# Kernel tuning notes

Hardware: AMD Instinct MI355X
Metric: run time of the kernel (lower is better)

Reference implementation:

```python
import jax, jax.numpy as jnp
import numpy as np

B, C, H, W = 8, 64, 256, 256
K = 3  # num_experts in CondConv2D


def setup_inputs() -> dict:
    key = jax.random.key(0)
    ks = jax.random.split(key, 10)
    s = 0.05
    return {
        "x":    jax.random.normal(ks[0], (B, C, H, W), jnp.float32),
        # CondConv2D #1: depthwise 5x5, pad 2, dil 1
        "w0":   jax.random.normal(ks[1], (K, C, 1, 5, 5), jnp.float32) * s,
        "b0":   jax.random.normal(ks[2], (C,), jnp.float32) * s,
        "r0_w": jax.random.normal(ks[3], (K, C), jnp.float32) * s,
        "r0_b": jnp.zeros((K,), jnp.float32),
        # CondConv2D #2: depthwise 7x7, pad 9, dil 3
        "w1":   jax.random.normal(ks[4], (K, C, 1, 7, 7), jnp.float32) * s,
        "b1":   jax.random.normal(ks[5], (C,), jnp.float32) * s,
        "r1_w": jax.random.normal(ks[6], (K, C), jnp.float32) * s,
        "r1_b": jnp.zeros((K,), jnp.float32),
        # conv1: 1x1 pointwise
        "wp":   jax.random.normal(ks[7], (C, C), jnp.float32) * s,
        "bp":   jnp.zeros((C,), jnp.float32),
    }


def cond_dwconv(x, weight, bias, rw, rb, pad, dil):
    """Per-sample expert-mixed depthwise conv (CondConv with groups=C).
    x: [B,C,H,W]; weight: [K,C,1,ks,ks]; rw: [K,C], rb: [K]."""
    b, c, h, w = x.shape
    pooled = x.mean(axis=(2, 3))                      # [B,C] adaptive avg pool to 1x1
    r = jax.nn.sigmoid(pooled @ rw.T + rb)            # [B,K] routing weights
    wk = jnp.einsum('bk,kcihw->bcihw', r, weight)     # [B,C,1,ks,ks] mixed kernels
    ksz = weight.shape[-1]
    # batch-folded grouped conv: fold B into channel/group dim
    out = jax.lax.conv_general_dilated(
        x.reshape(1, b * c, h, w),
        wk.reshape(b * c, 1, ksz, ksz),
        window_strides=(1, 1),
        padding=[(pad, pad), (pad, pad)],
        rhs_dilation=(dil, dil),
        feature_group_count=b * c,
        dimension_numbers=('NCHW', 'OIHW', 'NCHW'))
    return out.reshape(b, c, h, w) + bias[None, :, None, None]


def reference(x, w0, b0, r0_w, r0_b, w1, b1, r1_w, r1_b, wp, bp):
    attn = jax.nn.gelu(cond_dwconv(x, w0, b0, r0_w, r0_b, pad=2, dil=1), approximate=False)
    attn = jax.nn.gelu(cond_dwconv(attn, w1, b1, r1_w, r1_b, pad=9, dil=3), approximate=False)
    attn = jnp.einsum('bchw,oc->bohw', attn, wp) + bp[None, :, None, None]  # 1x1 conv
    return x * attn
```

## Files before the change

### kernel.cpp

```cpp
#include <hip/hip_runtime.h>
#include <hip/hip_fp16.h>

#define HW 65536
#define PW 256
#define C7S 168

__device__ __forceinline__ float gelu_f(float v) {
    float ax = fabsf(v) * 0.7071067811865476f;
    float t  = 1.0f / (1.0f + 0.3275911f * ax);
    float p  = t * (0.254829592f + t * (-0.284496736f + t * (1.421413741f
             + t * (-1.453152027f + t * 1.061405429f))));
    float e  = 1.0f - p * __expf(-ax * ax);
    e = copysignf(e, v);
    return 0.5f * v * (1.0f + e);
}

__device__ __forceinline__ unsigned pack2h(float a, float b) {
    __half2 h = __floats2half2_rn(a, b);
    return *reinterpret_cast<unsigned*>(&h);
}

__device__ __forceinline__ void unpack8(uint4 u, float* dst) {
    float2 f;
    f = __half22float2(*reinterpret_cast<__half2*>(&u.x)); dst[0] = f.x; dst[1] = f.y;
    f = __half22float2(*reinterpret_cast<__half2*>(&u.y)); dst[2] = f.x; dst[3] = f.y;
    f = __half22float2(*reinterpret_cast<__half2*>(&u.z)); dst[4] = f.x; dst[5] = f.y;
    f = __half22float2(*reinterpret_cast<__half2*>(&u.w)); dst[6] = f.x; dst[7] = f.y;
}

__device__ __forceinline__ float sgpr_f(float v) {
    union { float f; int i; } u;
    u.f = v;
    u.i = __builtin_amdgcn_readfirstlane(u.i);
    return u.f;
}

__device__ __forceinline__ void fma_mix_h(float& acc, float w, unsigned h2, int sel) {
    if (sel == 0)
        asm("v_fma_mix_f32 %0, %1, %2, %0 op_sel:[0,0,0] op_sel_hi:[0,1,0]"
            : "+v"(acc) : "v"(w), "v"(h2));
    else
        asm("v_fma_mix_f32 %0, %1, %2, %0 op_sel:[0,1,0] op_sel_hi:[0,1,0]"
            : "+v"(acc) : "v"(w), "v"(h2));
}

__global__ __launch_bounds__(256) void k_pool_x(const float* __restrict__ x,
                                                float* __restrict__ partial) {
    __shared__ float red[256];
    const int t = threadIdx.x;
    const int blk = blockIdx.x;
    const float* p = x + (size_t)blk * 16384;
    float s = 0.f;
    #pragma unroll
    for (int i = 0; i < 16; ++i) {
        float4 v = *reinterpret_cast<const float4*>(p + (i * 256 + t) * 4);
        s += v.x + v.y + v.z + v.w;
    }
    red[t] = s;
    __syncthreads();
    for (int off = 128; off > 0; off >>= 1) {
        if (t < off) red[t] += red[t + off];
        __syncthreads();
    }
    if (t == 0) partial[blk] = red[0];
}

__global__ __launch_bounds__(64) void k_route_mix(const float* __restrict__ partial,
                                                  const float* __restrict__ rw,
                                                  const float* __restrict__ rb,
                                                  const float* __restrict__ wexp,
                                                  float* __restrict__ wkout,
                                                  int taps, int parts) {
    __shared__ float pool_s[64];
    __shared__ float r_s[3];
    const int b = blockIdx.x, c = threadIdx.x;
    float s = 0.f;
    for (int q = 0; q < parts; ++q) s += partial[(b * 64 + c) * parts + q];
    pool_s[c] = s * (1.0f / 65536.0f);
    __syncthreads();
    if (c < 3) {
        float z = rb[c];
        #pragma unroll
        for (int i = 0; i < 64; ++i) z += pool_s[i] * rw[c * 64 + i];
        r_s[c] = 1.0f / (1.0f + expf(-z));
    }
    __syncthreads();
    const float r0 = r_s[0], r1 = r_s[1], r2 = r_s[2];
    for (int j = 0; j < taps; ++j) {
        wkout[(b * 64 + c) * taps + j] =
            r0 * wexp[(0 * 64 + c) * taps + j] +
            r1 * wexp[(1 * 64 + c) * taps + j] +
            r2 * wexp[(2 * 64 + c) * taps + j];
    }
}

__global__ __launch_bounds__(256) void k_conv5(const float* __restrict__ x,
                                               const float* __restrict__ wk,
                                               const float* __restrict__ bias,
                                               __half* __restrict__ attn0,
                                               float* __restrict__ tilesum) {
    __shared__ float red[256];
    const int blk = blockIdx.x;
    const int plane = blk >> 2;
    const int tile = blk & 3;
    const int c = plane & 63;
    const int oy0 = (tile >> 1) << 7;
    const int ox0 = (tile & 1) << 7;
    const int t = threadIdx.x;
    const int ox = ox0 + ((t & 15) << 3);
    const int oy = oy0 + ((t >> 4) << 3);
    const float* xp = x + (size_t)plane * HW;
    const float* wkp = wk + plane * 25;
    float w[25];
    #pragma unroll
    for (int i = 0; i < 25; ++i) w[i] = sgpr_f(wkp[i]);
    float acc[8][8];
    #pragma unroll
    for (int i = 0; i < 8; ++i)
        #pragma unroll
        for (int j = 0; j < 8; ++j) acc[i][j] = 0.f;

    #pragma unroll
    for (int r = 0; r < 12; ++r) {
        const int gy = oy - 2 + r;
        if (gy >= 0 && gy < 256) {
            const float* rp = xp + gy * PW + ox;
            float buf[16];
            float4 v;
            if (ox > 0) v = *reinterpret_cast<const float4*>(rp - 4);
            else        v = make_float4(0.f, 0.f, 0.f, 0.f);
            buf[0] = v.x; buf[1] = v.y; buf[2] = v.z; buf[3] = v.w;
            v = *reinterpret_cast<const float4*>(rp);
            buf[4] = v.x; buf[5] = v.y; buf[6] = v.z; buf[7] = v.w;
            v = *reinterpret_cast<const float4*>(rp + 4);
            buf[8] = v.x; buf[9] = v.y; buf[10] = v.z; buf[11] = v.w;
            if (ox < 248) v = *reinterpret_cast<const float4*>(rp + 8);
            else          v = make_float4(0.f, 0.f, 0.f, 0.f);
            buf[12] = v.x; buf[13] = v.y; buf[14] = v.z; buf[15] = v.w;
            #pragma unroll
            for (int i = 0; i < 8; ++i) {
                const int d = r - i;
                if (d >= 0 && d <= 4) {
                    #pragma unroll
                    for (int dx = 0; dx < 5; ++dx) {
                        const float wv = w[d * 5 + dx];
                        #pragma unroll
                        for (int j = 0; j < 8; ++j)
                            acc[i][j] += wv * buf[j + dx + 2];
                    }
                }
            }
        }
    }
    const float bs = bias[c];
    float lsum = 0.f;
    __half* op = attn0 + (size_t)plane * HW;
    #pragma unroll
    for (int i = 0; i < 8; ++i) {
        float g[8];
        #pragma unroll
        for (int j = 0; j < 8; ++j) {
            g[j] = gelu_f(acc[i][j] + bs);
            lsum += g[j];
        }
        uint4 st;
        st.x = pack2h(g[0], g[1]); st.y = pack2h(g[2], g[3]);
        st.z = pack2h(g[4], g[5]); st.w = pack2h(g[6], g[7]);
        *reinterpret_cast<uint4*>(op + (oy + i) * PW + ox) = st;
    }
    red[t] = lsum;
    __syncthreads();
    for (int off = 128; off > 0; off >>= 1) {
        if (t < off) red[t] += red[t + off];
        __syncthreads();
    }
    if (t == 0) tilesum[blk] = red[0];
}

__global__ __launch_bounds__(256) void k_conv7(const __half* __restrict__ a0,
                                               const float* __restrict__ wk,
                                               const float* __restrict__ bias,
                                               __half* __restrict__ attn1) {
    __shared__ __half lds[82 * C7S];
    const int blk = blockIdx.x;
    const int plane = blk >> 3;
    const int tile = blk & 7;
    const int c = plane & 63;
    const int oy0 = (tile >> 1) << 6;
    const int ox0 = (tile & 1) << 7;
    const int t = threadIdx.x;
    const __half* ap = a0 + (size_t)plane * HW;

    const uint4 z4 = make_uint4(0u, 0u, 0u, 0u);
    #pragma unroll
    for (int it = 0; it < 7; ++it) {
        const int idx = it * 256 + t;
        if (idx < 1722) {
            const int lr = idx / 21;
            const int c8 = idx - lr * 21;
            const int gy = oy0 - 9 + lr;
            const int gx = ox0 - 16 + (c8 << 3);
            uint4 v = z4;
            if ((unsigned)gy < 256u && (unsigned)gx < 256u)
                v = *reinterpret_cast<const uint4*>(ap + gy * PW + gx);
            *reinterpret_cast<uint4*>(&lds[lr * C7S + (c8 << 3)]) = v;
        }
    }

    float w[49];
    #pragma unroll
    for (int i = 0; i < 49; ++i) w[i] = sgpr_f(wk[plane * 49 + i]);
    __syncthreads();

    const int tx = t & 3, ty = t >> 2;
    const int ox = tx << 5;
    float acc[32];
    #pragma unroll
    for (int j = 0; j < 32; ++j) acc[j] = 0.f;

    #pragma unroll
    for (int dyi = 0; dyi < 7; ++dyi) {
        const int lr = ty + 3 * dyi;
        const __half* lp = &lds[lr * C7S + ox];
        unsigned hbuf[32];
        #pragma unroll
        for (int k = 0; k < 8; ++k)
            *reinterpret_cast<uint4*>(&hbuf[k << 2]) =
                *reinterpret_cast<const uint4*>(lp + (k << 3));
        #pragma unroll
        for (int dxi = 0; dxi < 7; ++dxi) {
            const float wv = w[dyi * 7 + dxi];
            const int o = 7 + 3 * dxi;
            #pragma unroll
            for (int j = 0; j < 32; ++j) {
                const int h = o + j;
                fma_mix_h(acc[j], wv, hbuf[h >> 1], h & 1);
            }
        }
    }

    const float bs = bias[c];
    __half* op = attn1 + (size_t)plane * HW + (size_t)(oy0 + ty) * PW + ox0 + ox;
    #pragma unroll
    for (int q = 0; q < 4; ++q) {
        float g[8];
        #pragma unroll
        for (int j = 0; j < 8; ++j) g[j] = gelu_f(acc[q * 8 + j] + bs);
        uint4 st;
        st.x = pack2h(g[0], g[1]); st.y = pack2h(g[2], g[3]);
        st.z = pack2h(g[4], g[5]); st.w = pack2h(g[6], g[7]);
        *reinterpret_cast<uint4*>(op + (q << 3)) = st;
    }
}

__global__ __launch_bounds__(256) void k_mix(const __half* __restrict__ attn1,
                                             const float* __restrict__ wpm,
                                             const float* __restrict__ bp,
                                             const float* __restrict__ x,
                                             float* __restrict__ out) {
    __shared__ __half A_s[64][256];
    __shared__ float wpT[64][64];
    const int t = threadIdx.x;
    const int blk = blockIdx.x;
    const int b = blk >> 8;
    const int p0g = (blk & 255) << 8;
    #pragma unroll
    for (int it = 0; it < 8; ++it) {
        const int ci = it * 256 + t;
        const int row = ci >> 5;
        const int off = (ci & 31) << 3;
        uint4 u = *reinterpret_cast<const uint4*>(attn1 + (size_t)(b * 64 + row) * HW + p0g + off);
        *reinterpret_cast<uint4*>(&A_s[row][off]) = u;
    }
    #pragma unroll
    for (int j = 0; j < 16; ++j) {
        const int idx = j * 256 + t;
        const int cc = idx & 63;
        const int oo = idx >> 6;
        wpT[cc][oo] = wpm[oo * 64 + cc];
    }
    __syncthreads();
    const int o0 = (t >> 5) << 3;
    const int p0 = (t & 31) << 3;
    float acc[8][8];
    #pragma unroll
    for (int i = 0; i < 8; ++i)
        #pragma unroll
        for (int j = 0; j < 8; ++j) acc[i][j] = 0.f;
    #pragma unroll 4
    for (int cc = 0; cc < 64; ++cc) {
        float4 wa = *reinterpret_cast<const float4*>(&wpT[cc][o0]);
        float4 wb = *reinterpret_cast<const float4*>(&wpT[cc][o0 + 4]);
        const float wv[8] = {wa.x, wa.y, wa.z, wa.w, wb.x, wb.y, wb.z, wb.w};
        float af[8];
        uint4 u = *reinterpret_cast<const uint4*>(&A_s[cc][p0]);
        unpack8(u, af);
        #pragma unroll
        for (int oo = 0; oo < 8; ++oo) {
            const float wvv = wv[oo];
            #pragma unroll
            for (int pp = 0; pp < 8; ++pp) acc[oo][pp] += wvv * af[pp];
        }
    }
    #pragma unroll
    for (int oo = 0; oo < 8; ++oo) {
        const int o = o0 + oo;
        const float bb = bp[o];
        const size_t base = (size_t)(b * 64 + o) * HW + p0g + p0;
        float4 x0 = *reinterpret_cast<const float4*>(x + base);
        float4 x1 = *reinterpret_cast<const float4*>(x + base + 4);
        float4 r0, r1;
        r0.x = x0.x * (acc[oo][0] + bb); r0.y = x0.y * (acc[oo][1] + bb);
        r0.z = x0.z * (acc[oo][2] + bb); r0.w = x0.w * (acc[oo][3] + bb);
        r1.x = x1.x * (acc[oo][4] + bb); r1.y = x1.y * (acc[oo][5] + bb);
        r1.z = x1.z * (acc[oo][6] + bb); r1.w = x1.w * (acc[oo][7] + bb);
        *reinterpret_cast<float4*>(out + base) = r0;
        *reinterpret_cast<float4*>(out + base + 4) = r1;
    }
}

extern "C" void kernel_launch(void* const* d_in, const int* in_sizes, int n_in,
                              void* d_out, int out_size, void* d_ws, size_t ws_size,
                              hipStream_t stream) {
    const float* x   = (const float*)d_in[0];
    const float* w0  = (const float*)d_in[1];
    const float* b0  = (const float*)d_in[2];
    const float* r0w = (const float*)d_in[3];
    const float* r0b = (const float*)d_in[4];
    const float* w1  = (const float*)d_in[5];
    const float* b1  = (const float*)d_in[6];
    const float* r1w = (const float*)d_in[7];
    const float* r1b = (const float*)d_in[8];
    const float* wpm = (const float*)d_in[9];
    const float* bp  = (const float*)d_in[10];
    float* out = (float*)d_out;

    char* ws = (char*)d_ws;
    __half* attn0   = (__half*)(ws);
    __half* attn1   = (__half*)(ws + 67108864);
    float* partial0 = (float*)(ws + 134217728);
    float* tilesum1 = (float*)(ws + 134217728 + 8192);
    float* wk0      = (float*)(ws + 134217728 + 16384);
    float* wk1      = (float*)(ws + 134217728 + 16384 + 51200);

    k_pool_x<<<2048, 256, 0, stream>>>(x, partial0);
    k_route_mix<<<8, 64, 0, stream>>>(partial0, r0w, r0b, w0, wk0, 25, 4);
    k_conv5<<<2048, 256, 0, stream>>>(x, wk0, b0, attn0, tilesum1);
    k_route_mix<<<8, 64, 0, stream>>>(tilesum1, r1w, r1b, w1, wk1, 49, 4);
    k_conv7<<<4096, 256, 0, stream>>>(attn0, wk1, b1, attn1);
    k_mix<<<2048, 256, 0, stream>>>(attn1, wpm, bp, x, out);
}
```

Before: 266.8 us.

## Fuse routing/kernel-mix into conv kernels and pad conv7 LDS row stride

Removes the two small k_route_mix launches. Each conv block now recomputes the routing sigmoid and its own mixed depthwise kernel in shared memory from the pooled partial sums. This saves launch overhead and the tiny serial kernels between the big ones, at the cost of redundant routing work and extra barriers in every block. The conv7 LDS tile is also restrided to 85 dwords per row with word-granular stores and loads, aimed at reducing bank conflicts, but it gives up 128-bit LDS accesses.

New measurement: 257.2 us. 3.6% less time.

```diff
diff --git a/kernel.cpp b/kernel.cpp
--- a/kernel.cpp
+++ b/kernel.cpp
@@ -3,7 +3,7 @@
 
 #define HW 65536
 #define PW 256
-#define C7S 168
+#define C7SD 85
 
 __device__ __forceinline__ float gelu_f(float v) {
     float ax = fabsf(v) * 0.7071067811865476f;
@@ -65,44 +65,50 @@
     if (t == 0) partial[blk] = red[0];
 }
 
-__global__ __launch_bounds__(64) void k_route_mix(const float* __restrict__ partial,
-                                                  const float* __restrict__ rw,
-                                                  const float* __restrict__ rb,
-                                                  const float* __restrict__ wexp,
-                                                  float* __restrict__ wkout,
-                                                  int taps, int parts) {
-    __shared__ float pool_s[64];
-    __shared__ float r_s[3];
-    const int b = blockIdx.x, c = threadIdx.x;
-    float s = 0.f;
-    for (int q = 0; q < parts; ++q) s += partial[(b * 64 + c) * parts + q];
-    pool_s[c] = s * (1.0f / 65536.0f);
-    __syncthreads();
-    if (c < 3) {
-        float z = rb[c];
-        #pragma unroll
-        for (int i = 0; i < 64; ++i) z += pool_s[i] * rw[c * 64 + i];
-        r_s[c] = 1.0f / (1.0f + expf(-z));
-    }
-    __syncthreads();
-    const float r0 = r_s[0], r1 = r_s[1], r2 = r_s[2];
-    for (int j = 0; j < taps; ++j) {
-        wkout[(b * 64 + c) * taps + j] =
-            r0 * wexp[(0 * 64 + c) * taps + j] +
-            r1 * wexp[(1 * 64 + c) * taps + j] +
-            r2 * wexp[(2 * 64 + c) * taps + j];
-    }
+__device__ __forceinline__ void route_block(const float* __restrict__ partial,
+                                            const float* __restrict__ rw,
+                                            const float* __restrict__ rb,
+                                            const float* __restrict__ wexp,
+                                            int b, int c, int taps, int t,
+                                            float* pool_s, float* r_s, float* w_s) {
+    if (t < 64) {
+        float s = 0.f;
+        #pragma unroll
+        for (int q = 0; q < 4; ++q) s += partial[(b * 64 + t) * 4 + q];
+        pool_s[t] = s * (1.0f / 65536.0f);
+    }
+    __syncthreads();
+    if (t < 3) {
+        float z = rb[t];
+        #pragma unroll
+        for (int i = 0; i < 64; ++i) z += pool_s[i] * rw[t * 64 + i];
+        r_s[t] = 1.0f / (1.0f + expf(-z));
+    }
+    __syncthreads();
+    if (t < taps) {
+        w_s[t] = r_s[0] * wexp[(0 * 64 + c) * taps + t] +
+                 r_s[1] * wexp[(1 * 64 + c) * taps + t] +
+                 r_s[2] * wexp[(2 * 64 + c) * taps + t];
+    }
+    __syncthreads();
 }
 
 __global__ __launch_bounds__(256) void k_conv5(const float* __restrict__ x,
-                                               const float* __restrict__ wk,
+                                               const float* __restrict__ partial,
+                                               const float* __restrict__ rw,
+                                               const float* __restrict__ rb,
+                                               const float* __restrict__ wexp,
                                                const float* __restrict__ bias,
                                                __half* __restrict__ attn0,
                                                float* __restrict__ tilesum) {
     __shared__ float red[256];
+    __shared__ float pool_s[64];
+    __shared__ float r_s[3];
+    __shared__ float w_s[25];
     const int blk = blockIdx.x;
     const int plane = blk >> 2;
     const int tile = blk & 3;
+    const int b = plane >> 6;
     const int c = plane & 63;
     const int oy0 = (tile >> 1) << 7;
     const int ox0 = (tile & 1) << 7;
@@ -110,10 +116,12 @@
     const int ox = ox0 + ((t & 15) << 3);
     const int oy = oy0 + ((t >> 4) << 3);
     const float* xp = x + (size_t)plane * HW;
-    const float* wkp = wk + plane * 25;
+
+    route_block(partial, rw, rb, wexp, b, c, 25, t, pool_s, r_s, w_s);
     float w[25];
     #pragma unroll
-    for (int i = 0; i < 25; ++i) w[i] = sgpr_f(wkp[i]);
+    for (int i = 0; i < 25; ++i) w[i] = sgpr_f(w_s[i]);
+
     float acc[8][8];
     #pragma unroll
     for (int i = 0; i < 8; ++i)
@@ -178,13 +186,20 @@
 }
 
 __global__ __launch_bounds__(256) void k_conv7(const __half* __restrict__ a0,
-                                               const float* __restrict__ wk,
+                                               const float* __restrict__ tilesum,
+                                               const float* __restrict__ rw,
+                                               const float* __restrict__ rb,
+                                               const float* __restrict__ wexp,
                                                const float* __restrict__ bias,
                                                __half* __restrict__ attn1) {
-    __shared__ __half lds[82 * C7S];
+    __shared__ unsigned lds[82 * C7SD];
+    __shared__ float pool_s[64];
+    __shared__ float r_s[3];
+    __shared__ float w_s[49];
     const int blk = blockIdx.x;
     const int plane = blk >> 3;
     const int tile = blk & 7;
+    const int b = plane >> 6;
     const int c = plane & 63;
     const int oy0 = (tile >> 1) << 6;
     const int ox0 = (tile & 1) << 7;
@@ -203,13 +218,15 @@
             uint4 v = z4;
             if ((unsigned)gy < 256u && (unsigned)gx < 256u)
                 v = *reinterpret_cast<const uint4*>(ap + gy * PW + gx);
-            *reinterpret_cast<uint4*>(&lds[lr * C7S + (c8 << 3)]) = v;
-        }
-    }
-
+            unsigned* wp = &lds[lr * C7SD + (c8 << 2)];
+            wp[0] = v.x; wp[1] = v.y; wp[2] = v.z; wp[3] = v.w;
+        }
+    }
+
+    route_block(tilesum, rw, rb, wexp, b, c, 49, t, pool_s, r_s, w_s);
     float w[49];
     #pragma unroll
-    for (int i = 0; i < 49; ++i) w[i] = sgpr_f(wk[plane * 49 + i]);
+    for (int i = 0; i < 49; ++i) w[i] = sgpr_f(w_s[i]);
     __syncthreads();
 
     const int tx = t & 3, ty = t >> 2;
@@ -221,12 +238,10 @@
     #pragma unroll
     for (int dyi = 0; dyi < 7; ++dyi) {
         const int lr = ty + 3 * dyi;
-        const __half* lp = &lds[lr * C7S + ox];
+        const unsigned* lp = &lds[lr * C7SD + (tx << 4)];
         unsigned hbuf[32];
         #pragma unroll
-        for (int k = 0; k < 8; ++k)
-            *reinterpret_cast<uint4*>(&hbuf[k << 2]) =
-                *reinterpret_cast<const uint4*>(lp + (k << 3));
+        for (int i = 0; i < 32; ++i) hbuf[i] = lp[i];
         #pragma unroll
         for (int dxi = 0; dxi < 7; ++dxi) {
             const float wv = w[dyi * 7 + dxi];
@@ -340,13 +355,9 @@
     __half* attn1   = (__half*)(ws + 67108864);
     float* partial0 = (float*)(ws + 134217728);
     float* tilesum1 = (float*)(ws + 134217728 + 8192);
-    float* wk0      = (float*)(ws + 134217728 + 16384);
-    float* wk1      = (float*)(ws + 134217728 + 16384 + 51200);
 
     k_pool_x<<<2048, 256, 0, stream>>>(x, partial0);
-    k_route_mix<<<8, 64, 0, stream>>>(partial0, r0w, r0b, w0, wk0, 25, 4);
-    k_conv5<<<2048, 256, 0, stream>>>(x, wk0, b0, attn0, tilesum1);
-    k_route_mix<<<8, 64, 0, stream>>>(tilesum1, r1w, r1b, w1, wk1, 49, 4);
-    k_conv7<<<4096, 256, 0, stream>>>(attn0, wk1, b1, attn1);
+    k_conv5<<<2048, 256, 0, stream>>>(x, partial0, r0w, r0b, w0, b0, attn0, tilesum1);
+    k_conv7<<<4096, 256, 0, stream>>>(attn0, tilesum1, r1w, r1b, w1, b1, attn1);
     k_mix<<<2048, 256, 0, stream>>>(attn1, wpm, bp, x, out);
 }
```
